# Optimization experiments

Hardware: AMD Instinct MI355X
Metric: run time of the kernel (lower is better)

## Reference

```python
import jax, jax.numpy as jnp
import numpy as np

BLOCK_SIZE = 32
STRIDE = 16
DIM = 128


def setup_inputs() -> dict:
    key = jax.random.key(0)
    ks = jax.random.split(key, 6)
    B, N, C = 8, 16384, DIM
    x = jax.random.normal(ks[0], (B, N, C), dtype=jnp.float32)
    pos = jax.random.normal(ks[1], (1, BLOCK_SIZE, C), dtype=jnp.float32) * 0.02
    # torch Linear stores W:(out,in); we store transposed (in,out) for x @ W
    fan_in1 = C * BLOCK_SIZE
    W1 = jax.random.uniform(ks[2], (fan_in1, 2 * C), dtype=jnp.float32,
                            minval=-1.0, maxval=1.0) / jnp.sqrt(fan_in1)
    b1 = jax.random.uniform(ks[3], (2 * C,), dtype=jnp.float32,
                            minval=-1.0, maxval=1.0) / jnp.sqrt(fan_in1)
    fan_in2 = 2 * C
    W2 = jax.random.uniform(ks[4], (fan_in2, C), dtype=jnp.float32,
                            minval=-1.0, maxval=1.0) / jnp.sqrt(fan_in2)
    b2 = jax.random.uniform(ks[5], (C,), dtype=jnp.float32,
                            minval=-1.0, maxval=1.0) / jnp.sqrt(fan_in2)
    return {"x": x, "pos": pos, "W1": W1, "b1": b1, "W2": W2, "b2": b2}


def reference(x, pos, W1, b1, W2, b2):
    B, N, C = x.shape
    l, d = BLOCK_SIZE, STRIDE
    if N < l:  # static shapes -> plain Python branch is fine
        return jnp.mean(x, axis=1, keepdims=True)
    num_blocks = (N - l) // d + 1
    # overlapping sliding-window gather: (nb, l) token indices
    idx = jnp.arange(num_blocks)[:, None] * d + jnp.arange(l)[None, :]
    blocks = x[:, idx, :] + pos[None]            # (B, nb, l, C)
    blocks = blocks.reshape(B, num_blocks, l * C)  # (B, nb, l*C)
    h = jax.nn.gelu(blocks @ W1 + b1, approximate=False)  # exact erf GELU (torch default)
    return h @ W2 + b2                           # (B, nb, C)
```

## Files before the change

kernel.cpp:

```cpp
#include <hip/hip_runtime.h>
#include <hip/hip_bf16.h>
#include <math.h>


typedef __attribute__((ext_vector_type(8))) short short8;
typedef __attribute__((ext_vector_type(4))) float f4;

#define OFF_BT   0u
#define OFF_W2T  (2u << 20)
#define OFF_PART ((2u << 20) + (64u << 10))
#define OFF_BIAS ((2u << 20) + (128u << 10))
#define OFF_P    (4u << 20)

static __device__ __forceinline__ unsigned short f2bf(float f) {
  union { float f; unsigned u; } v; v.f = f;
  return (unsigned short)((v.u + 0x7FFFu + ((v.u >> 16) & 1u)) >> 16);
}
static __device__ __forceinline__ float bf2f(unsigned short h) {
  union { unsigned u; float f; } v; v.u = ((unsigned)h) << 16;
  return v.f;
}
static __device__ __forceinline__ void gload_lds16(const void* g, void* l) {
  __builtin_amdgcn_global_load_lds(
      (const __attribute__((address_space(1))) void*)g,
      (__attribute__((address_space(3))) void*)l, 16, 0, 0);
}

__global__ __launch_bounds__(256) void k_prep(const float* __restrict__ W1,
                                              const float* __restrict__ pos,
                                              const float* __restrict__ W2,
                                              unsigned short* __restrict__ Bt,
                                              unsigned short* __restrict__ W2t,
                                              float* __restrict__ part) {
  __shared__ float T[64][65];
  const int w = blockIdx.x;
  const int t = threadIdx.x;
  if (w >= 256) {
    const int n = w - 256;
    W2t[n * 256 + t] = f2bf(W2[t * 128 + n]);
    return;
  }
  const int h = w >> 7, rem = w & 127, kt = rem >> 2, nt = rem & 3;
  const int krow0 = h * 2048 + kt * 64, col0 = nt * 64;
  const int lr = t >> 2, lc = (t & 3) * 16;
  const float* src = W1 + (size_t)(krow0 + lr) * 256 + col0 + lc;
#pragma unroll
  for (int i = 0; i < 4; ++i) {
    f4 v = *(const f4*)(src + i * 4);
#pragma unroll
    for (int q = 0; q < 4; ++q) T[lr][lc + i * 4 + q] = v[q];
  }
  __syncthreads();
  if (t < 64) {
    float s = 0.f;
#pragma unroll 8
    for (int k = 0; k < 64; ++k) s += T[k][t] * pos[krow0 + k];
    part[(h * 32 + kt) * 256 + col0 + t] = s;
  }
  const int nl = t >> 2, kc = (t & 3) * 16;
  short8 o0, o1;
#pragma unroll
  for (int i = 0; i < 8; ++i) o0[i] = (short)f2bf(T[kc + i][nl]);
#pragma unroll
  for (int i = 0; i < 8; ++i) o1[i] = (short)f2bf(T[kc + 8 + i][nl]);
  unsigned short* dst = Bt + (size_t)(256 * h + col0 + nl) * 2048 + kt * 64 + kc;
  *(short8*)dst = o0;
  *(short8*)(dst + 8) = o1;
}

__global__ __launch_bounds__(256) void k_bias(const float* __restrict__ b1,
                                              const float* __restrict__ part,
                                              float* __restrict__ bias) {
  int n = threadIdx.x;
  float s = b1[n];
#pragma unroll 8
  for (int g = 0; g < 64; ++g) s += part[g * 256 + n];
  bias[n] = s;
}

__global__ __launch_bounds__(512) void k_gemm(const float* __restrict__ X,
                                              const unsigned short* __restrict__ Bt,
                                              unsigned short* __restrict__ P) {
  __shared__ __align__(16) char lds[2][49152];
  const int orig = blockIdx.x;
  const int wg = (orig & 7) * 32 + (orig >> 3);
  const int mt = wg >> 3;
  const int nt = (wg >> 2) & 1;
  const int ksp = wg & 3;
  const int m0 = mt * 256, n0 = nt * 256, k0 = ksp * 512;
  const int t = threadIdx.x;
  const int wid = t >> 6, lane = t & 63;
  const int wr = wid >> 1, wc = wid & 1;

  f4 acc[4][8];
#pragma unroll
  for (int m = 0; m < 4; ++m)
#pragma unroll
    for (int n = 0; n < 8; ++n) acc[m][n] = f4{0.f, 0.f, 0.f, 0.f};

#define ISSUE(BUF, KT)                                                     \
  do {                                                                     \
    const int kf = k0 + (KT) * 32;                                         \
    _Pragma("unroll") for (int ii = 0; ii < 4; ++ii) {                     \
      const int s = ii * 512 + t;                                          \
      const int row = s >> 3, c8 = s & 7;                                  \
      gload_lds16(X + (size_t)(m0 + row) * 2048 + kf +                     \
                      ((c8 ^ (row & 7)) << 2),                             \
                  &lds[BUF][ii * 8192 + wid * 1024]);                      \
    }                                                                      \
    _Pragma("unroll") for (int ii = 0; ii < 2; ++ii) {                     \
      const int s = ii * 512 + t;                                          \
      const int row = s >> 2, c4 = s & 3;                                  \
      gload_lds16(Bt + (size_t)(n0 + row) * 2048 + kf +                    \
                      ((c4 ^ (row & 3)) << 3),                             \
                  &lds[BUF][32768 + ii * 8192 + wid * 1024]);              \
    }                                                                      \
  } while (0)

#define COMPUTE(BUF)                                                       \
  do {                                                                     \
    const float* Ab = (const float*)&lds[BUF][0];                          \
    const unsigned short* Bb = (const unsigned short*)&lds[BUF][32768];    \
    short8 af[4], bfv[8];                                                  \
    const int q = lane >> 4;                                               \
    _Pragma("unroll") for (int m = 0; m < 4; ++m) {                        \
      const int row = wr * 64 + m * 16 + (lane & 15);                      \
      const int e = row & 7;                                               \
      f4 lo = *(const f4*)(Ab + row * 32 + (((2 * q) ^ e) << 2));          \
      f4 hi = *(const f4*)(Ab + row * 32 + (((2 * q + 1) ^ e) << 2));      \
      union { short8 s8; unsigned u[4]; } pk;                              \
      asm("v_cvt_pk_bf16_f32 %0, %1, %2" : "=v"(pk.u[0])                   \
          : "v"(lo[0]), "v"(lo[1]));                                       \
      asm("v_cvt_pk_bf16_f32 %0, %1, %2" : "=v"(pk.u[1])                   \
          : "v"(lo[2]), "v"(lo[3]));                                       \
      asm("v_cvt_pk_bf16_f32 %0, %1, %2" : "=v"(pk.u[2])                   \
          : "v"(hi[0]), "v"(hi[1]));                                       \
      asm("v_cvt_pk_bf16_f32 %0, %1, %2" : "=v"(pk.u[3])                   \
          : "v"(hi[2]), "v"(hi[3]));                                       \
      af[m] = pk.s8;                                                       \
    }                                                                      \
    _Pragma("unroll") for (int n = 0; n < 8; ++n) {                        \
      const int row = wc * 128 + n * 16 + (lane & 15);                     \
      bfv[n] = *(const short8*)((const unsigned short*)Bb + row * 32 +     \
                                ((q ^ (row & 3)) << 3));                   \
    }                                                                      \
    __builtin_amdgcn_s_setprio(1);                                         \
    _Pragma("unroll") for (int m = 0; m < 4; ++m)                          \
      _Pragma("unroll") for (int n = 0; n < 8; ++n)                        \
        acc[m][n] = __builtin_amdgcn_mfma_f32_16x16x32_bf16(               \
            af[m], bfv[n], acc[m][n], 0, 0, 0);                            \
    __builtin_amdgcn_s_setprio(0);                                         \
  } while (0)

  ISSUE(0, 0);
  ISSUE(1, 1);
  __builtin_amdgcn_sched_barrier(0);
  asm volatile("s_waitcnt vmcnt(6)" ::: "memory");
  __builtin_amdgcn_s_barrier();
  __builtin_amdgcn_sched_barrier(0);

#pragma unroll 2
  for (int kt = 0; kt < 16; ++kt) {
    COMPUTE(kt & 1);
    __builtin_amdgcn_sched_barrier(0);
    __builtin_amdgcn_s_barrier();
    __builtin_amdgcn_sched_barrier(0);
    if (kt < 14) {
      ISSUE(kt & 1, kt + 2);
      __builtin_amdgcn_sched_barrier(0);
      asm volatile("s_waitcnt vmcnt(6)" ::: "memory");
      __builtin_amdgcn_s_barrier();
      __builtin_amdgcn_sched_barrier(0);
    } else if (kt == 14) {
      asm volatile("s_waitcnt vmcnt(0)" ::: "memory");
      __builtin_amdgcn_s_barrier();
      __builtin_amdgcn_sched_barrier(0);
    }
  }
#undef ISSUE
#undef COMPUTE

  unsigned short* Pp = P + (size_t)ksp * (8192 * 512);
  const int mb = m0 + wr * 64, nb = n0 + wc * 128;
#pragma unroll
  for (int m = 0; m < 4; ++m)
#pragma unroll
    for (int n = 0; n < 8; ++n) {
      const int row0 = mb + m * 16 + ((lane >> 4) << 2);
      const int col = nb + n * 16 + (lane & 15);
#pragma unroll
      for (int r = 0; r < 4; ++r)
        Pp[(size_t)(row0 + r) * 512 + col] = f2bf(acc[m][n][r]);
    }
}

__global__ __launch_bounds__(256) void k_comb(const unsigned short* __restrict__ P,
                                              const unsigned short* __restrict__ W2t,
                                              const float* __restrict__ bias,
                                              const float* __restrict__ b2,
                                              float* __restrict__ out) {
  __shared__ unsigned short W2s[128 * 256];
  __shared__ unsigned short Hs[32 * 256];
  const int wg = blockIdx.x;
  const int b = wg >> 5, jt = wg & 31;
  const int j0 = jt * 32;
  const int t = threadIdx.x;

  {
    const int row = t >> 1, halfc = (t & 1) * 128;
    const unsigned short* src = W2t + row * 256 + halfc;
    const int cbw = halfc >> 3;
#pragma unroll
    for (int i = 0; i < 16; ++i) {
      short8 v = *(const short8*)(src + i * 8);
      const int c = (cbw + i) ^ (row & 7);
      *(short8*)&W2s[row * 256 + c * 8] = v;
    }
  }
  {
    const int r = t >> 3, seg = t & 7;
    const int j = j0 + r;
    const size_t m = (size_t)b * 1024 + j;
    const size_t mp1 = (j < 1023) ? m + 1 : m;
    const float* bs = bias + seg * 32;
    const int cbh = seg * 4;
#pragma unroll
    for (int i = 0; i < 4; ++i) {
      float f0[8];
#pragma unroll
      for (int q = 0; q < 8; ++q) f0[q] = bs[i * 8 + q];
#pragma unroll
      for (int ksp = 0; ksp < 4; ++ksp) {
        const unsigned short* Pk = P + (size_t)ksp * (8192 * 512);
        short8 v0 = *(const short8*)(Pk + m * 512 + seg * 32 + i * 8);
        short8 v1 = *(const short8*)(Pk + mp1 * 512 + 256 + seg * 32 + i * 8);
#pragma unroll
        for (int q = 0; q < 8; ++q)
          f0[q] += bf2f((unsigned short)v0[q]) + bf2f((unsigned short)v1[q]);
      }
      short8 pk;
#pragma unroll
      for (int q = 0; q < 8; ++q) {
        float g = 0.5f * f0[q] * (1.f + erff(f0[q] * 0.70710678118f));
        pk[q] = (short)f2bf(g);
      }
      const int c = (cbh + i) ^ (r & 7);
      *(short8*)&Hs[r * 256 + c * 8] = pk;
    }
  }
  __syncthreads();

  const int wid = t >> 6, lane = t & 63;
  f4 acc[2][2];
#pragma unroll
  for (int i = 0; i < 2; ++i)
#pragma unroll
    for (int j = 0; j < 2; ++j) acc[i][j] = f4{0.f, 0.f, 0.f, 0.f};

#pragma unroll
  for (int ks = 0; ks < 8; ++ks) {
    short8 af[2], bfr[2];
    const int cc = ks * 4 + (lane >> 4);
#pragma unroll
    for (int f = 0; f < 2; ++f) {
      const int ra = f * 16 + (lane & 15);
      af[f] = *(const short8*)&Hs[ra * 256 + ((cc ^ (ra & 7)) << 3)];
      const int rb = wid * 32 + f * 16 + (lane & 15);
      bfr[f] = *(const short8*)&W2s[rb * 256 + ((cc ^ (rb & 7)) << 3)];
    }
#pragma unroll
    for (int i = 0; i < 2; ++i)
#pragma unroll
      for (int j = 0; j < 2; ++j)
        acc[i][j] = __builtin_amdgcn_mfma_f32_16x16x32_bf16(af[i], bfr[j],
                                                            acc[i][j], 0, 0, 0);
  }
#pragma unroll
  for (int i = 0; i < 2; ++i)
#pragma unroll
    for (int j = 0; j < 2; ++j) {
      const int row0 = i * 16 + ((lane >> 4) << 2);
      const int col = wid * 32 + j * 16 + (lane & 15);
      const float bb = b2[col];
#pragma unroll
      for (int r = 0; r < 4; ++r) {
        const int jj = j0 + row0 + r;
        if (jj < 1023)
          out[((size_t)b * 1023 + jj) * 128 + col] = acc[i][j][r] + bb;
      }
    }
}

extern "C" void kernel_launch(void* const* d_in, const int* in_sizes, int n_in,
                              void* d_out, int out_size, void* d_ws, size_t ws_size,
                              hipStream_t stream) {
  const float* x   = (const float*)d_in[0];
  const float* pos = (const float*)d_in[1];
  const float* W1  = (const float*)d_in[2];
  const float* b1  = (const float*)d_in[3];
  const float* W2  = (const float*)d_in[4];
  const float* b2  = (const float*)d_in[5];
  float* out = (float*)d_out;
  char* ws = (char*)d_ws;
  unsigned short* Bt  = (unsigned short*)(ws + OFF_BT);
  unsigned short* W2t = (unsigned short*)(ws + OFF_W2T);
  float* part         = (float*)(ws + OFF_PART);
  float* bias         = (float*)(ws + OFF_BIAS);
  unsigned short* P   = (unsigned short*)(ws + OFF_P);

  k_prep<<<384, 256, 0, stream>>>(W1, pos, W2, Bt, W2t, part);
  k_bias<<<1, 256, 0, stream>>>(b1, part, bias);
  k_gemm<<<256, 512, 0, stream>>>(x, Bt, P);
  k_comb<<<256, 256, 0, stream>>>(P, W2t, bias, b2, out);
}
```

Baseline: 58.62 us.

## Retile GEMM to full-N tiles, triple-buffer LDS, fold bias kernel into GEMM

The GEMM now gives each workgroup a 128-row M tile covering all 512 output columns instead of 256x256. The B swizzle changes to match. LDS goes from double to triple buffering, with the next load issued before compute and one barrier per iteration. The separate one-block bias-reduction kernel is removed: every GEMM workgroup recomputes the bias redundantly, and the combine kernel stages it in LDS. This removes one launch and may overlap loads better, at the cost of more LDS (lower occupancy), redundant bias writes and a changed A/B reuse ratio.

```diff
diff --git a/kernel.cpp b/kernel.cpp
--- a/kernel.cpp
+++ b/kernel.cpp
@@ -68,29 +68,21 @@
   *(short8*)(dst + 8) = o1;
 }
 
-__global__ __launch_bounds__(256) void k_bias(const float* __restrict__ b1,
-                                              const float* __restrict__ part,
-                                              float* __restrict__ bias) {
-  int n = threadIdx.x;
-  float s = b1[n];
-#pragma unroll 8
-  for (int g = 0; g < 64; ++g) s += part[g * 256 + n];
-  bias[n] = s;
-}
-
 __global__ __launch_bounds__(512) void k_gemm(const float* __restrict__ X,
                                               const unsigned short* __restrict__ Bt,
+                                              const float* __restrict__ part,
+                                              const float* __restrict__ b1,
+                                              float* __restrict__ biasG,
                                               unsigned short* __restrict__ P) {
-  __shared__ __align__(16) char lds[2][49152];
+  __shared__ __align__(16) char lds[3][49152];
   const int orig = blockIdx.x;
-  const int wg = (orig & 7) * 32 + (orig >> 3);
-  const int mt = wg >> 3;
-  const int nt = (wg >> 2) & 1;
-  const int ksp = wg & 3;
-  const int m0 = mt * 256, n0 = nt * 256, k0 = ksp * 512;
+  const int wgid = (orig & 7) * 32 + (orig >> 3);
+  const int mt = wgid >> 2;
+  const int ksp = wgid & 3;
+  const int m0 = mt * 128, k0 = ksp * 512;
   const int t = threadIdx.x;
   const int wid = t >> 6, lane = t & 63;
-  const int wr = wid >> 1, wc = wid & 1;
+  const int wr = wid >> 2, wc = wid & 3;
 
   f4 acc[4][8];
 #pragma unroll
@@ -101,26 +93,26 @@
 #define ISSUE(BUF, KT)                                                     \
   do {                                                                     \
     const int kf = k0 + (KT) * 32;                                         \
-    _Pragma("unroll") for (int ii = 0; ii < 4; ++ii) {                     \
+    _Pragma("unroll") for (int ii = 0; ii < 2; ++ii) {                     \
       const int s = ii * 512 + t;                                          \
       const int row = s >> 3, c8 = s & 7;                                  \
       gload_lds16(X + (size_t)(m0 + row) * 2048 + kf +                     \
                       ((c8 ^ (row & 7)) << 2),                             \
                   &lds[BUF][ii * 8192 + wid * 1024]);                      \
     }                                                                      \
-    _Pragma("unroll") for (int ii = 0; ii < 2; ++ii) {                     \
+    _Pragma("unroll") for (int ii = 0; ii < 4; ++ii) {                     \
       const int s = ii * 512 + t;                                          \
       const int row = s >> 2, c4 = s & 3;                                  \
-      gload_lds16(Bt + (size_t)(n0 + row) * 2048 + kf +                    \
-                      ((c4 ^ (row & 3)) << 3),                             \
-                  &lds[BUF][32768 + ii * 8192 + wid * 1024]);              \
+      gload_lds16(Bt + (size_t)row * 2048 + kf +                           \
+                      ((c4 ^ ((row >> 1) & 3)) << 3),                      \
+                  &lds[BUF][16384 + ii * 8192 + wid * 1024]);              \
     }                                                                      \
   } while (0)
 
 #define COMPUTE(BUF)                                                       \
   do {                                                                     \
     const float* Ab = (const float*)&lds[BUF][0];                          \
-    const unsigned short* Bb = (const unsigned short*)&lds[BUF][32768];    \
+    const unsigned short* Bb = (const unsigned short*)&lds[BUF][16384];    \
     short8 af[4], bfv[8];                                                  \
     const int q = lane >> 4;                                               \
     _Pragma("unroll") for (int m = 0; m < 4; ++m) {                        \
@@ -141,8 +133,8 @@
     }                                                                      \
     _Pragma("unroll") for (int n = 0; n < 8; ++n) {                        \
       const int row = wc * 128 + n * 16 + (lane & 15);                     \
-      bfv[n] = *(const short8*)((const unsigned short*)Bb + row * 32 +     \
-                                ((q ^ (row & 3)) << 3));                   \
+      bfv[n] = *(const short8*)(Bb + row * 32 +                            \
+                                ((q ^ ((row >> 1) & 3)) << 3));            \
     }                                                                      \
     __builtin_amdgcn_s_setprio(1);                                         \
     _Pragma("unroll") for (int m = 0; m < 4; ++m)                          \
@@ -159,29 +151,29 @@
   __builtin_amdgcn_s_barrier();
   __builtin_amdgcn_sched_barrier(0);
 
-#pragma unroll 2
   for (int kt = 0; kt < 16; ++kt) {
-    COMPUTE(kt & 1);
+    if (kt < 14) ISSUE((kt + 2) % 3, kt + 2);
+    COMPUTE(kt % 3);
     __builtin_amdgcn_sched_barrier(0);
-    __builtin_amdgcn_s_barrier();
-    __builtin_amdgcn_sched_barrier(0);
-    if (kt < 14) {
-      ISSUE(kt & 1, kt + 2);
-      __builtin_amdgcn_sched_barrier(0);
-      asm volatile("s_waitcnt vmcnt(6)" ::: "memory");
+    if (kt < 15) {
+      if (kt < 14) asm volatile("s_waitcnt vmcnt(6)" ::: "memory");
+      else         asm volatile("s_waitcnt vmcnt(0)" ::: "memory");
       __builtin_amdgcn_s_barrier();
       __builtin_amdgcn_sched_barrier(0);
-    } else if (kt == 14) {
-      asm volatile("s_waitcnt vmcnt(0)" ::: "memory");
-      __builtin_amdgcn_s_barrier();
-      __builtin_amdgcn_sched_barrier(0);
     }
   }
 #undef ISSUE
 #undef COMPUTE
 
+  if (t < 256) {
+    float s = b1[t];
+#pragma unroll 8
+    for (int g = 0; g < 64; ++g) s += part[g * 256 + t];
+    biasG[t] = s;
+  }
+
   unsigned short* Pp = P + (size_t)ksp * (8192 * 512);
-  const int mb = m0 + wr * 64, nb = n0 + wc * 128;
+  const int mb = m0 + wr * 64, nb = wc * 128;
 #pragma unroll
   for (int m = 0; m < 4; ++m)
 #pragma unroll
@@ -196,16 +188,18 @@
 
 __global__ __launch_bounds__(256) void k_comb(const unsigned short* __restrict__ P,
                                               const unsigned short* __restrict__ W2t,
-                                              const float* __restrict__ bias,
+                                              const float* __restrict__ biasG,
                                               const float* __restrict__ b2,
                                               float* __restrict__ out) {
   __shared__ unsigned short W2s[128 * 256];
   __shared__ unsigned short Hs[32 * 256];
+  __shared__ float biasS[256];
   const int wg = blockIdx.x;
   const int b = wg >> 5, jt = wg & 31;
   const int j0 = jt * 32;
   const int t = threadIdx.x;
 
+  biasS[t] = biasG[t];
   {
     const int row = t >> 1, halfc = (t & 1) * 128;
     const unsigned short* src = W2t + row * 256 + halfc;
@@ -217,12 +211,13 @@
       *(short8*)&W2s[row * 256 + c * 8] = v;
     }
   }
+  __syncthreads();
   {
     const int r = t >> 3, seg = t & 7;
     const int j = j0 + r;
     const size_t m = (size_t)b * 1024 + j;
     const size_t mp1 = (j < 1023) ? m + 1 : m;
-    const float* bs = bias + seg * 32;
+    const float* bs = biasS + seg * 32;
     const int cbh = seg * 4;
 #pragma unroll
     for (int i = 0; i < 4; ++i) {
@@ -305,11 +300,10 @@
   unsigned short* Bt  = (unsigned short*)(ws + OFF_BT);
   unsigned short* W2t = (unsigned short*)(ws + OFF_W2T);
   float* part         = (float*)(ws + OFF_PART);
-  float* bias         = (float*)(ws + OFF_BIAS);
+  float* biasG        = (float*)(ws + OFF_BIAS);
   unsigned short* P   = (unsigned short*)(ws + OFF_P);
 
   k_prep<<<384, 256, 0, stream>>>(W1, pos, W2, Bt, W2t, part);
-  k_bias<<<1, 256, 0, stream>>>(b1, part, bias);
-  k_gemm<<<256, 512, 0, stream>>>(x, Bt, P);
-  k_comb<<<256, 256, 0, stream>>>(P, W2t, bias, b2, out);
-}
+  k_gemm<<<256, 512, 0, stream>>>(x, Bt, part, b1, biasG, P);
+  k_comb<<<256, 256, 0, stream>>>(P, W2t, biasG, b2, out);
+}
```

Result: faster. 50.66 us (-13.6%).
